# Kernel optimization log

Hardware: AMD Instinct MI355X
Metric: run time of the kernel (lower is better)

## Reference

```python
import jax, jax.numpy as jnp
import numpy as np

B, N1, N2 = 2, 2048, 8192
IN_F, OUT_F = 128, 64
ALPHA = 0.2
NEG = -9e15


def setup_inputs() -> dict:
    key = jax.random.key(0)
    ks = jax.random.split(key, 8)
    stdv = 1.0 / np.sqrt(OUT_F)
    x = jax.random.normal(ks[0], (B, N2, IN_F), dtype=jnp.float32)
    adj = (jax.random.uniform(ks[1], (B, N1, N2)) < 0.05).astype(jnp.float32)
    u = lambda k, shp: jax.random.uniform(k, shp, minval=-stdv, maxval=stdv, dtype=jnp.float32)
    W2 = u(ks[2], (IN_F, OUT_F))
    W3 = u(ks[3], (OUT_F, OUT_F))
    a = u(ks[4], (2 * OUT_F, 1))
    a2 = u(ks[5], (2 * OUT_F, 1))
    word_ctx = u(ks[6], (OUT_F,))
    return {"x": x, "adj": adj, "W2": W2, "W3": W3, "a": a, "a2": a2, "word_ctx": word_ctx}


def reference(x, adj, W2, W3, a, a2, word_ctx):
    F_out = W2.shape[1]
    x4 = jnp.einsum('bnf,fo->bno', x, W2)            # [B, N2, F] node features for attention
    mask = adj > 0                                     # [B, N1, N2]
    # --- stage 1: edge-level attention over member nodes (softmax over N2) ---
    # pair score = leakyrelu([word_ctx, x4_j] @ a); independent of hyperedge index i
    a_q, a_x = a[:F_out, 0], a[F_out:, 0]
    s1 = jax.nn.leaky_relu(jnp.dot(word_ctx, a_q) + x4 @ a_x, ALPHA)  # [B, N2]
    e1 = jnp.where(mask, s1[:, None, :], NEG)          # [B, N1, N2]
    att_edge = jax.nn.softmax(e1, axis=2)
    edge = jnp.einsum('bij,bjf->bif', att_edge, x4)    # [B, N1, F]
    edge4 = jnp.einsum('bif,fo->bio', edge, W3)        # [B, N1, F]
    # --- stage 2: node-level attention over incident hyperedges (softmax over N1) ---
    a2_x, a2_e = a2[:F_out, 0], a2[F_out:, 0]
    s2 = jax.nn.leaky_relu((edge4 @ a2_e)[:, :, None] + (x4 @ a2_x)[:, None, :], ALPHA)  # [B, N1, N2]
    e2 = jnp.where(mask, s2, NEG)
    att_node = jax.nn.softmax(jnp.transpose(e2, (0, 2, 1)), axis=2)  # [B, N2, N1]
    node = jnp.einsum('bji,bif->bjf', att_node, edge4)               # [B, N2, F]
    return node, edge
```

## Files before the change

### kernel.cpp

```cpp
#include <hip/hip_runtime.h>
#include <stdint.h>

#define NB 2
#define N1 2048
#define N2 8192
#define INF_ 128
#define F 64
#define ALPHA 0.2f
#define CAP_E 640
#define CAP_N 192

__device__ __forceinline__ float bf2f(unsigned short u) {
    return __uint_as_float((unsigned int)u << 16);
}
__device__ __forceinline__ unsigned short f2bf(float f) {
    unsigned int u = __float_as_uint(f);
    u += 0x7FFF + ((u >> 16) & 1);
    return (unsigned short)(u >> 16);
}
__device__ __forceinline__ float blo(unsigned int d) { return __uint_as_float(d << 16); }
__device__ __forceinline__ float bhi(unsigned int d) { return __uint_as_float(d & 0xFFFF0000u); }

__global__ __launch_bounds__(256) void k_mask_csr(
    const float4* __restrict__ adj4, uint64_t* __restrict__ bits,
    uint16_t* __restrict__ idxE, int* __restrict__ cntE)
{
    __shared__ uint64_t sBits[128];
    __shared__ uint16_t sIdx[CAP_E];
    __shared__ int      sCnt[4];
    int tid  = threadIdx.x;
    int lane = tid & 63;
    int w    = tid >> 6;
    int row  = blockIdx.x;
    int b    = row >> 11;

    const float4* ar = adj4 + (size_t)row * (N2 / 4) + (size_t)w * 512 + lane;
    float4 v[8];
    #pragma unroll
    for (int it = 0; it < 8; ++it) v[it] = ar[it * 64];
    int cnt = 0;
    #pragma unroll
    for (int it = 0; it < 8; ++it) {
        unsigned long long m0 = __ballot(v[it].x != 0.0f);
        unsigned long long m1 = __ballot(v[it].y != 0.0f);
        unsigned long long m2 = __ballot(v[it].z != 0.0f);
        unsigned long long m3 = __ballot(v[it].w != 0.0f);
        if (lane == 0) {
            uint64_t* o = &sBits[w * 32 + it * 4];
            o[0] = m0; o[1] = m1; o[2] = m2; o[3] = m3;
        }
        cnt += (int)__popcll(m0) + (int)__popcll(m1)
             + (int)__popcll(m2) + (int)__popcll(m3);
    }
    if (lane == 0) sCnt[w] = cnt;
    __syncthreads();

    int c0 = sCnt[0], c1 = sCnt[1], c2 = sCnt[2], c3 = sCnt[3];
    int base = (w > 0 ? c0 : 0) + (w > 1 ? c1 : 0) + (w > 2 ? c2 : 0);
    int total = c0 + c1 + c2 + c3;
    uint64_t lmask = (1ull << lane) - 1;
    #pragma unroll
    for (int k = 0; k < 32; ++k) {
        int wi = w * 32 + k;
        uint64_t m = sBits[wi];
        if ((m >> lane) & 1) {
            int pos = base + (int)__popcll(m & lmask);
            sIdx[pos] = (uint16_t)(((wi >> 2) << 8) + (lane << 2) + (wi & 3));
        }
        base += (int)__popcll(m);
    }
    int n = total;
    int padded = (n + 15) & ~15;
    if (padded > CAP_E) padded = CAP_E;
    if (w == 3) {
        uint16_t sent = (uint16_t)((NB - b) * N2);
        if (n + lane < padded) sIdx[n + lane] = sent;
    }
    __syncthreads();

    uint64_t* bw = bits + (size_t)row * (N2 / 64);
    if (tid < 128) bw[tid] = sBits[tid];
    const uint32_t* s32 = (const uint32_t*)sIdx;
    uint32_t* o32 = (uint32_t*)(idxE + (size_t)row * CAP_E);
    for (int d = tid; 2 * d < padded; d += 256) o32[d] = s32[d];
    if (tid == 0) cntE[row] = n;
}

union XU {
    struct { float w2s[INF_ * F]; float4 xs4[64 * 32]; } x;
    struct {
        uint16_t idxn[64][194];
        int      pre[8][64];
        int      cnt[64];
    } t;
};

__global__ __launch_bounds__(512) void k_x4t(
    const float* __restrict__ x, const float* __restrict__ W2,
    const float* __restrict__ a, const float* __restrict__ a2,
    const float* __restrict__ wctx,
    uint16_t* __restrict__ y16, float* __restrict__ w1, float* __restrict__ q,
    const uint64_t* __restrict__ bits,
    uint16_t* __restrict__ idxN, int* __restrict__ cntN)
{
    __shared__ XU su;
    int tid  = threadIdx.x;
    int lane = tid & 63;
    int w    = tid >> 6;

    if (blockIdx.x < 256) {
        for (int idx = tid; idx < INF_ * F; idx += 512) su.x.w2s[idx] = W2[idx];
        if (blockIdx.x == 0) {
            if (tid < F) y16[(size_t)NB * N2 * F + tid] = 0;
            if (tid == 0) w1[NB * N2] = 0.f;
        }
        {
            const float4* xg4 = (const float4*)(x + (size_t)blockIdx.x * 64 * INF_);
            int r  = tid >> 3;
            int c0 = (tid & 7) * 4;
            #pragma unroll
            for (int i = 0; i < 4; ++i)
                su.x.xs4[r * 32 + c0 + i] = xg4[r * 32 + c0 + i];
        }
        float cpart = wctx[lane] * a[lane];
        #pragma unroll
        for (int s = 32; s; s >>= 1) cpart += __shfl_xor(cpart, s);
        float ax  = a[64 + lane];
        float a2x = a2[lane];
        __syncthreads();

        float acc[8] = {0.f, 0.f, 0.f, 0.f, 0.f, 0.f, 0.f, 0.f};
        for (int k4 = 0; k4 < 32; ++k4) {
            float wk0 = su.x.w2s[(4 * k4 + 0) * F + lane];
            float wk1 = su.x.w2s[(4 * k4 + 1) * F + lane];
            float wk2 = su.x.w2s[(4 * k4 + 2) * F + lane];
            float wk3 = su.x.w2s[(4 * k4 + 3) * F + lane];
            #pragma unroll
            for (int r = 0; r < 8; ++r) {
                float4 xv = su.x.xs4[(8 * w + r) * 32 + k4];
                acc[r] = fmaf(xv.x, wk0, acc[r]);
                acc[r] = fmaf(xv.y, wk1, acc[r]);
                acc[r] = fmaf(xv.z, wk2, acc[r]);
                acc[r] = fmaf(xv.w, wk3, acc[r]);
            }
        }
        int row0 = blockIdx.x * 64 + 8 * w;
        #pragma unroll
        for (int r = 0; r < 8; ++r) {
            float acc_ = acc[r];
            float r1 = acc_ * ax, r2 = acc_ * a2x;
            #pragma unroll
            for (int s = 32; s; s >>= 1) { r1 += __shfl_xor(r1, s); r2 += __shfl_xor(r2, s); }
            float s1 = cpart + r1;
            s1 = fmaxf(s1, ALPHA * s1);
            float wv1 = __expf(s1);
            y16[(size_t)(row0 + r) * F + lane] = f2bf(wv1 * acc_);
            if (lane == 0) { w1[row0 + r] = wv1; q[row0 + r] = r2; }
        }
    } else {
        int blk = blockIdx.x - 256;
        int b  = blk >> 7;
        int jw = blk & 127;
        const uint64_t Mtab[6] = {0x00000000FFFFFFFFull, 0x0000FFFF0000FFFFull,
                                  0x00FF00FF00FF00FFull, 0x0F0F0F0F0F0F0F0Full,
                                  0x3333333333333333ull, 0x5555555555555555ull};
        uint64_t wd[4];
        #pragma unroll
        for (int t = 0; t < 4; ++t) {
            int ib = w * 4 + t;
            uint64_t xv = bits[((size_t)(b * N1 + ib * 64 + lane)) * (N2 / 64) + jw];
            #pragma unroll
            for (int st = 0; st < 6; ++st) {
                int s = 32 >> st;
                uint64_t M = Mtab[st];
                uint64_t yy = (uint64_t)__shfl_xor((unsigned long long)xv, s);
                xv = ((lane & s) == 0) ? ((xv & M) | ((yy & M) << s))
                                       : ((xv & ~M) | ((yy & ~M) >> s));
            }
            wd[t] = xv;
        }
        int myc = 0;
        #pragma unroll
        for (int t = 0; t < 4; ++t) myc += (int)__popcll(wd[t]);
        su.t.pre[w][lane] = myc;
        __syncthreads();
        int base = 0, total = 0;
        #pragma unroll
        for (int ww = 0; ww < 8; ++ww) {
            int c = su.t.pre[ww][lane];
            if (ww < w) base += c;
            total += c;
        }
        int n = total < CAP_N ? total : CAP_N;
        if (w == 0) su.t.cnt[lane] = n;

        uint16_t* sr = su.t.idxn[lane];
        int off = base;
        #pragma unroll
        for (int t = 0; t < 4; ++t) {
            uint64_t m = wd[t];
            int ibase = (w * 4 + t) << 6;
            while (m) {
                int ii = __builtin_ctzll(m); m &= m - 1;
                if (off < CAP_N) sr[off] = (uint16_t)(ibase + ii);
                ++off;
            }
        }
        int jp = jw * 64 + lane;
        int j  = ((jp >> 8) << 8) + ((jp & 63) << 2) + ((jp >> 6) & 3);
        int rowOut = b * N2 + j;
        if (w == 7) {
            int padded = (n + 15) & ~15;
            if (padded > CAP_N) padded = CAP_N;
            uint16_t sent = (uint16_t)((NB - b) * N1);
            for (int o = n; o < padded; ++o) sr[o] = sent;
            cntN[rowOut] = n;
        }
        __syncthreads();
        int jbase = b * N2 + ((jw >> 2) << 8) + (jw & 3);
        for (int rr = 0; rr < 8; ++rr) {
            int r = w * 8 + rr;
            int n_r = su.t.cnt[r];
            int padded_r = (n_r + 15) & ~15;
            if (padded_r > CAP_N) padded_r = CAP_N;
            int rowOut_r = jbase + r * 4;
            uint32_t* dst = (uint32_t*)(idxN + (size_t)rowOut_r * CAP_N);
            const uint32_t* src = (const uint32_t*)su.t.idxn[r];
            for (int d = lane; 2 * d < padded_r; d += 64) dst[d] = src[d];
        }
    }
}

__global__ __launch_bounds__(256) void kD(
    const uint16_t* __restrict__ idxE, const int* __restrict__ cntE,
    const uint16_t* __restrict__ y16, const float* __restrict__ w1,
    const float* __restrict__ W3, const float* __restrict__ a2,
    float* __restrict__ out_edge, uint16_t* __restrict__ e16, float* __restrict__ p)
{
    __shared__ float  w3s[F * F];
    __shared__ float4 scr4[4][16];
    int tid  = threadIdx.x;
    int lane = tid & 63;
    int w    = tid >> 6;
    for (int idx = tid; idx < F * F; idx += 256) w3s[idx] = W3[idx];
    if (blockIdx.x == 0 && tid == 0) p[NB * N1] = -1e30f;
    __syncthreads();
    int g   = lane >> 3;
    int sub = lane & 7;
    int row = (blockIdx.x * 256 + tid) >> 6;
    int b = row >> 11;
    const uint4* yb = (const uint4*)y16 + (size_t)b * N2 * 8;
    const float* w1b = w1 + (size_t)b * N2;
    const uint16_t* ix = idxE + (size_t)row * CAP_E;
    int n = cntE[row];
    int padded = (n + 15) & ~15;
    if (padded > CAP_E) padded = CAP_E;
    float4 aA = make_float4(0.f, 0.f, 0.f, 0.f);
    float4 aB = make_float4(0.f, 0.f, 0.f, 0.f);
    float zl = 0.f, zl4 = 0.f;
    int t = 0;
    for (; t + 64 <= padded; t += 64) {
        int myj = ix[t + lane];
        zl += w1b[myj];
        #pragma unroll
        for (int s = 0; s < 8; ++s) {
            int jv = __shfl(myj, 8 * s + g);
            uint4 v = yb[(size_t)jv * 8 + sub];
            aA.x += blo(v.x); aA.y += bhi(v.x);
            aA.z += blo(v.y); aA.w += bhi(v.y);
            aB.x += blo(v.z); aB.y += bhi(v.z);
            aB.z += blo(v.w); aB.w += bhi(v.w);
        }
    }
    for (; t < padded; t += 16) {
        int myj = ix[t + (lane & 15)];
        zl4 += w1b[myj];
        #pragma unroll
        for (int s = 0; s < 2; ++s) {
            int jv = __shfl(myj, 8 * s + g);
            uint4 v = yb[(size_t)jv * 8 + sub];
            aA.x += blo(v.x); aA.y += bhi(v.x);
            aA.z += blo(v.y); aA.w += bhi(v.y);
            aB.x += blo(v.z); aB.y += bhi(v.z);
            aB.z += blo(v.w); aB.w += bhi(v.w);
        }
    }
    #pragma unroll
    for (int s2 = 8; s2 <= 32; s2 <<= 1) {
        aA.x += __shfl_xor(aA.x, s2); aA.y += __shfl_xor(aA.y, s2);
        aA.z += __shfl_xor(aA.z, s2); aA.w += __shfl_xor(aA.w, s2);
        aB.x += __shfl_xor(aB.x, s2); aB.y += __shfl_xor(aB.y, s2);
        aB.z += __shfl_xor(aB.z, s2); aB.w += __shfl_xor(aB.w, s2);
    }
    float zc = zl + 0.25f * zl4;
    #pragma unroll
    for (int s2 = 32; s2; s2 >>= 1) zc += __shfl_xor(zc, s2);
    float inv = 1.f / zc;
    float4 evA = make_float4(aA.x * inv, aA.y * inv, aA.z * inv, aA.w * inv);
    float4 evB = make_float4(aB.x * inv, aB.y * inv, aB.z * inv, aB.w * inv);
    if (lane < 8) {
        float4* o4 = (float4*)out_edge + (size_t)row * 16;
        o4[2 * lane]     = evA;
        o4[2 * lane + 1] = evB;
        scr4[w][2 * lane]     = evA;
        scr4[w][2 * lane + 1] = evB;
    }
    float ev = ((const float*)scr4[w])[lane];
    float a2e = a2[64 + lane];
    float acc4 = 0.f;
    #pragma unroll 8
    for (int gg = 0; gg < 64; ++gg) acc4 += __shfl(ev, gg) * w3s[gg * F + lane];
    e16[(size_t)row * F + lane] = f2bf(acc4);
    float r = acc4 * a2e;
    #pragma unroll
    for (int s2 = 32; s2; s2 >>= 1) r += __shfl_xor(r, s2);
    if (lane == 0) p[row] = r;
}

__global__ __launch_bounds__(256) void kE(
    const uint16_t* __restrict__ idxN, const int* __restrict__ cntN,
    const uint16_t* __restrict__ e16, const float* __restrict__ p,
    const float* __restrict__ q, float* __restrict__ out_node)
{
    int lane = threadIdx.x & 63;
    int g   = lane >> 3;
    int sub = lane & 7;
    int gw = (blockIdx.x * blockDim.x + threadIdx.x) >> 6;
    int nw = (gridDim.x * blockDim.x) >> 6;
    for (int row = gw; row < NB * N2; row += nw) {
        int b = row >> 13;
        const uint4*  eb = (const uint4*)e16 + (size_t)b * N1 * 8;
        const float*  pb = p + b * N1;
        const uint16_t* ix = idxN + (size_t)row * CAP_N;
        float qj = q[row];
        int n = cntN[row];
        int padded = (n + 15) & ~15;
        if (padded > CAP_N) padded = CAP_N;
        float4 aA = make_float4(0.f, 0.f, 0.f, 0.f);
        float4 aB = make_float4(0.f, 0.f, 0.f, 0.f);
        float zl = 0.f, zl4 = 0.f;
        int t = 0;
        for (; t + 64 <= padded; t += 64) {
            int myi = ix[t + lane];
            float sc = pb[myi] + qj;
            sc = fmaxf(sc, ALPHA * sc);
            float wl = __expf(sc);
            zl += wl;
            #pragma unroll
            for (int s = 0; s < 8; ++s) {
                int iv   = __shfl(myi, 8 * s + g);
                float wv = __shfl(wl,  8 * s + g);
                uint4 v = eb[(size_t)iv * 8 + sub];
                aA.x = fmaf(wv, blo(v.x), aA.x); aA.y = fmaf(wv, bhi(v.x), aA.y);
                aA.z = fmaf(wv, blo(v.y), aA.z); aA.w = fmaf(wv, bhi(v.y), aA.w);
                aB.x = fmaf(wv, blo(v.z), aB.x); aB.y = fmaf(wv, bhi(v.z), aB.y);
                aB.z = fmaf(wv, blo(v.w), aB.z); aB.w = fmaf(wv, bhi(v.w), aB.w);
            }
        }
        for (; t < padded; t += 16) {
            int myi = ix[t + (lane & 15)];
            float sc = pb[myi] + qj;
            sc = fmaxf(sc, ALPHA * sc);
            float wl = __expf(sc);
            zl4 += wl;
            #pragma unroll
            for (int s = 0; s < 2; ++s) {
                int iv   = __shfl(myi, 8 * s + g);
                float wv = __shfl(wl,  8 * s + g);
                uint4 v = eb[(size_t)iv * 8 + sub];
                aA.x = fmaf(wv, blo(v.x), aA.x); aA.y = fmaf(wv, bhi(v.x), aA.y);
                aA.z = fmaf(wv, blo(v.y), aA.z); aA.w = fmaf(wv, bhi(v.y), aA.w);
                aB.x = fmaf(wv, blo(v.z), aB.x); aB.y = fmaf(wv, bhi(v.z), aB.y);
                aB.z = fmaf(wv, blo(v.w), aB.z); aB.w = fmaf(wv, bhi(v.w), aB.w);
            }
        }
        #pragma unroll
        for (int s2 = 8; s2 <= 32; s2 <<= 1) {
            aA.x += __shfl_xor(aA.x, s2); aA.y += __shfl_xor(aA.y, s2);
            aA.z += __shfl_xor(aA.z, s2); aA.w += __shfl_xor(aA.w, s2);
            aB.x += __shfl_xor(aB.x, s2); aB.y += __shfl_xor(aB.y, s2);
            aB.z += __shfl_xor(aB.z, s2); aB.w += __shfl_xor(aB.w, s2);
        }
        float zc = zl + 0.25f * zl4;
        #pragma unroll
        for (int s2 = 32; s2; s2 >>= 1) zc += __shfl_xor(zc, s2);
        float inv = 1.f / zc;
        if (lane < 8) {
            float4* o4 = (float4*)out_node + (size_t)row * 16;
            o4[2 * lane]     = make_float4(aA.x * inv, aA.y * inv, aA.z * inv, aA.w * inv);
            o4[2 * lane + 1] = make_float4(aB.x * inv, aB.y * inv, aB.z * inv, aB.w * inv);
        }
    }
}

extern "C" void kernel_launch(void* const* d_in, const int* in_sizes, int n_in,
                              void* d_out, int out_size, void* d_ws, size_t ws_size,
                              hipStream_t stream)
{
    const float* x    = (const float*)d_in[0];
    const float* adj  = (const float*)d_in[1];
    const float* W2   = (const float*)d_in[2];
    const float* W3   = (const float*)d_in[3];
    const float* a    = (const float*)d_in[4];
    const float* a2   = (const float*)d_in[5];
    const float* wctx = (const float*)d_in[6];

    float* out      = (float*)d_out;
    float* node_out = out;
    float* edge_out = out + (size_t)NB * N2 * F;

    char* basep = (char*)d_ws;
    size_t o = 0;
    uint16_t* y16 = (uint16_t*)(basep + o);
    o += (size_t)(NB * N2 + 1) * F * 2;        o = (o + 255) & ~(size_t)255;
    float* w1 = (float*)(basep + o);
    o += (size_t)(NB * N2 + 4) * 4;            o = (o + 255) & ~(size_t)255;
    float* q = (float*)(basep + o);
    o += (size_t)NB * N2 * 4;                  o = (o + 255) & ~(size_t)255;
    uint16_t* e16 = (uint16_t*)(basep + o);
    o += (size_t)(NB * N1 + 1) * F * 2;        o = (o + 255) & ~(size_t)255;
    float* p = (float*)(basep + o);
    o += (size_t)(NB * N1 + 4) * 4;            o = (o + 255) & ~(size_t)255;
    uint64_t* bits = (uint64_t*)(basep + o);
    o += (size_t)NB * N1 * (N2 / 64) * 8;
    int* cntE = (int*)(basep + o);             o += (size_t)NB * N1 * 4;
    int* cntN = (int*)(basep + o);             o += (size_t)NB * N2 * 4;
    uint16_t* idxE = (uint16_t*)(basep + o);   o += (size_t)NB * N1 * CAP_E * 2;
    uint16_t* idxN = (uint16_t*)(basep + o);

    hipLaunchKernelGGL(k_mask_csr, dim3(NB * N1), dim3(256), 0, stream,
                       (const float4*)adj, bits, idxE, cntE);
    hipLaunchKernelGGL(k_x4t, dim3(512), dim3(512), 0, stream,
                       x, W2, a, a2, wctx, y16, w1, q, bits, idxN, cntN);
    hipLaunchKernelGGL(kD, dim3(NB * N1 / 4), dim3(256), 0, stream,
                       idxE, cntE, y16, w1, W3, a2, edge_out, e16, p);
    hipLaunchKernelGGL(kE, dim3(4096), dim3(256), 0, stream,
                       idxN, cntN, e16, p, q, node_out);
}
```

Baseline: 88.08 us.

## Split each edge row's gather across two waves and store W3 as bf16

In kD, each hyperedge row is now handled by two wavefronts that take alternating 64-element chunks of the member list. Their partial sums and normalisers are combined through shared memory, and the first wave of the pair finishes the W3 projection. The grid doubles so each block covers two rows instead of four. W3 is held in LDS as bf16, halving its shared footprint at some cost in precision. The aim is more parallelism and latency hiding on the gather, paid for with an extra barrier and an idle half-pair during the epilogue.

```diff
diff --git a/kernel.cpp b/kernel.cpp
--- a/kernel.cpp
+++ b/kernel.cpp
@@ -237,29 +237,32 @@
     const float* __restrict__ W3, const float* __restrict__ a2,
     float* __restrict__ out_edge, uint16_t* __restrict__ e16, float* __restrict__ p)
 {
-    __shared__ float  w3s[F * F];
-    __shared__ float4 scr4[4][16];
+    __shared__ uint16_t w3h[F * F];
+    __shared__ float4   scr[4][16];
+    __shared__ float    zred[4];
     int tid  = threadIdx.x;
     int lane = tid & 63;
     int w    = tid >> 6;
-    for (int idx = tid; idx < F * F; idx += 256) w3s[idx] = W3[idx];
+    for (int idx = tid; idx < F * F; idx += 256) w3h[idx] = f2bf(W3[idx]);
     if (blockIdx.x == 0 && tid == 0) p[NB * N1] = -1e30f;
     __syncthreads();
-    int g   = lane >> 3;
-    int sub = lane & 7;
-    int row = (blockIdx.x * 256 + tid) >> 6;
+
+    int row  = blockIdx.x * 2 + (w >> 1);
+    int half = w & 1;
     int b = row >> 11;
     const uint4* yb = (const uint4*)y16 + (size_t)b * N2 * 8;
     const float* w1b = w1 + (size_t)b * N2;
     const uint16_t* ix = idxE + (size_t)row * CAP_E;
+    int g   = lane >> 3;
+    int sub = lane & 7;
     int n = cntE[row];
     int padded = (n + 15) & ~15;
     if (padded > CAP_E) padded = CAP_E;
+    int fullEnd = padded & ~63;
     float4 aA = make_float4(0.f, 0.f, 0.f, 0.f);
     float4 aB = make_float4(0.f, 0.f, 0.f, 0.f);
     float zl = 0.f, zl4 = 0.f;
-    int t = 0;
-    for (; t + 64 <= padded; t += 64) {
+    for (int t = 64 * half; t + 64 <= fullEnd; t += 128) {
         int myj = ix[t + lane];
         zl += w1b[myj];
         #pragma unroll
@@ -272,17 +275,19 @@
             aB.z += blo(v.w); aB.w += bhi(v.w);
         }
     }
-    for (; t < padded; t += 16) {
-        int myj = ix[t + (lane & 15)];
-        zl4 += w1b[myj];
-        #pragma unroll
-        for (int s = 0; s < 2; ++s) {
-            int jv = __shfl(myj, 8 * s + g);
-            uint4 v = yb[(size_t)jv * 8 + sub];
-            aA.x += blo(v.x); aA.y += bhi(v.x);
-            aA.z += blo(v.y); aA.w += bhi(v.y);
-            aB.x += blo(v.z); aB.y += bhi(v.z);
-            aB.z += blo(v.w); aB.w += bhi(v.w);
+    if (half == 1) {
+        for (int t = fullEnd; t < padded; t += 16) {
+            int myj = ix[t + (lane & 15)];
+            zl4 += w1b[myj];
+            #pragma unroll
+            for (int s = 0; s < 2; ++s) {
+                int jv = __shfl(myj, 8 * s + g);
+                uint4 v = yb[(size_t)jv * 8 + sub];
+                aA.x += blo(v.x); aA.y += bhi(v.x);
+                aA.z += blo(v.y); aA.w += bhi(v.y);
+                aB.x += blo(v.z); aB.y += bhi(v.z);
+                aB.z += blo(v.w); aB.w += bhi(v.w);
+            }
         }
     }
     #pragma unroll
@@ -295,26 +300,32 @@
     float zc = zl + 0.25f * zl4;
     #pragma unroll
     for (int s2 = 32; s2; s2 >>= 1) zc += __shfl_xor(zc, s2);
-    float inv = 1.f / zc;
-    float4 evA = make_float4(aA.x * inv, aA.y * inv, aA.z * inv, aA.w * inv);
-    float4 evB = make_float4(aB.x * inv, aB.y * inv, aB.z * inv, aB.w * inv);
-    if (lane < 8) {
-        float4* o4 = (float4*)out_edge + (size_t)row * 16;
-        o4[2 * lane]     = evA;
-        o4[2 * lane + 1] = evB;
-        scr4[w][2 * lane]     = evA;
-        scr4[w][2 * lane + 1] = evB;
-    }
-    float ev = ((const float*)scr4[w])[lane];
-    float a2e = a2[64 + lane];
-    float acc4 = 0.f;
-    #pragma unroll 8
-    for (int gg = 0; gg < 64; ++gg) acc4 += __shfl(ev, gg) * w3s[gg * F + lane];
-    e16[(size_t)row * F + lane] = f2bf(acc4);
-    float r = acc4 * a2e;
-    #pragma unroll
-    for (int s2 = 32; s2; s2 >>= 1) r += __shfl_xor(r, s2);
-    if (lane == 0) p[row] = r;
+    if (lane < 8) { scr[w][2 * lane] = aA; scr[w][2 * lane + 1] = aB; }
+    if (lane == 0) zred[w] = zc;
+    __syncthreads();
+
+    if (half == 0) {
+        float z = zred[w] + zred[w + 1];
+        float inv = 1.f / z;
+        if (lane < 16) {
+            float4 m0 = scr[w][lane], m1 = scr[w + 1][lane];
+            float4 ev = make_float4((m0.x + m1.x) * inv, (m0.y + m1.y) * inv,
+                                    (m0.z + m1.z) * inv, (m0.w + m1.w) * inv);
+            ((float4*)out_edge)[(size_t)row * 16 + lane] = ev;
+            scr[w][lane] = ev;
+        }
+        float ev = ((const float*)scr[w])[lane];
+        float a2e = a2[64 + lane];
+        float acc4 = 0.f;
+        #pragma unroll 8
+        for (int gg = 0; gg < 64; ++gg)
+            acc4 += __shfl(ev, gg) * bf2f(w3h[gg * F + lane]);
+        e16[(size_t)row * F + lane] = f2bf(acc4);
+        float r = acc4 * a2e;
+        #pragma unroll
+        for (int s2 = 32; s2; s2 >>= 1) r += __shfl_xor(r, s2);
+        if (lane == 0) p[row] = r;
+    }
 }
 
 __global__ __launch_bounds__(256) void kE(
@@ -432,7 +443,7 @@
                        (const float4*)adj, bits, idxE, cntE);
     hipLaunchKernelGGL(k_x4t, dim3(512), dim3(512), 0, stream,
                        x, W2, a, a2, wctx, y16, w1, q, bits, idxN, cntN);
-    hipLaunchKernelGGL(kD, dim3(NB * N1 / 4), dim3(256), 0, stream,
+    hipLaunchKernelGGL(kD, dim3(NB * N1 / 2), dim3(256), 0, stream,
                        idxE, cntE, y16, w1, W3, a2, edge_out, e16, p);
     hipLaunchKernelGGL(kE, dim3(4096), dim3(256), 0, stream,
                        idxN, cntN, e16, p, q, node_out);
```

Result: slower. 90.08 us (+2.3%).
